# Kernel tuning notes

Hardware: AMD Instinct MI355X
Metric: run time of the kernel (lower is better)

## Reference

```python
import jax, jax.numpy as jnp
import numpy as np

N_PFAS, N_GW, N_SW = 20000, 100000, 20000
D_IN, D_OUT = 64, 128
E_PG, E_GP, E_SP, E_PS = 1600000, 1600000, 400000, 400000


def setup_inputs() -> dict:
    key = jax.random.key(0)
    ks = jax.random.split(key, 32)
    nrm = lambda k, shp, s=1.0: jax.random.normal(k, shp, jnp.float32) * s
    W = 0.05  # weight init scale
    inp = {
        # node features
        "x_pfas": nrm(ks[0], (N_PFAS, D_IN)),
        "x_gw": nrm(ks[1], (N_GW, D_IN)),
        "x_sw": nrm(ks[2], (N_SW, D_IN)),
        # edge indices per relation (src, dst)
        "ei_pg_src": jax.random.randint(ks[3], (E_PG,), 0, N_PFAS),
        "ei_pg_dst": jax.random.randint(ks[4], (E_PG,), 0, N_GW),
        "ei_gp_src": jax.random.randint(ks[5], (E_GP,), 0, N_GW),
        "ei_gp_dst": jax.random.randint(ks[6], (E_GP,), 0, N_PFAS),
        "ei_sp_src": jax.random.randint(ks[7], (E_SP,), 0, N_SW),
        "ei_sp_dst": jax.random.randint(ks[8], (E_SP,), 0, N_PFAS),
        "ei_ps_src": jax.random.randint(ks[9], (E_PS,), 0, N_PFAS),
        "ei_ps_dst": jax.random.randint(ks[10], (E_PS,), 0, N_SW),
        # SAGEConv params per relation: lin_l (neighbors, with bias), lin_r (root, no bias)
        "Wl_pg": nrm(ks[11], (D_IN, D_OUT), W), "Wr_pg": nrm(ks[12], (D_IN, D_OUT), W), "b_pg": jnp.zeros((D_OUT,), jnp.float32),
        "Wl_gp": nrm(ks[13], (D_IN, D_OUT), W), "Wr_gp": nrm(ks[14], (D_IN, D_OUT), W), "b_gp": jnp.zeros((D_OUT,), jnp.float32),
        "Wl_sp": nrm(ks[15], (D_IN, D_OUT), W), "Wr_sp": nrm(ks[16], (D_IN, D_OUT), W), "b_sp": jnp.zeros((D_OUT,), jnp.float32),
        "Wl_ps": nrm(ks[17], (D_IN, D_OUT), W), "Wr_ps": nrm(ks[18], (D_IN, D_OUT), W), "b_ps": jnp.zeros((D_OUT,), jnp.float32),
        # final linear head + PReLU
        "W_lin": nrm(ks[19], (D_OUT, 1), W), "b_lin": jnp.zeros((1,), jnp.float32),
        "alpha": jnp.full((1,), 0.25, jnp.float32),
    }
    return inp


def _sage(x_src, x_dst, src, dst, Wl, Wr, b, n_dst):
    # PyG SAGEConv: out = lin_l(mean_{j in N(i)} x_j) + lin_r(x_i)
    msg = x_src[src]                                   # [E, D_in] gather
    agg = jax.ops.segment_sum(msg, dst, num_segments=n_dst)        # [n_dst, D_in]
    cnt = jax.ops.segment_sum(jnp.ones(src.shape, x_src.dtype), dst, num_segments=n_dst)
    mean = agg / jnp.maximum(cnt, 1.0)[:, None]
    return mean @ Wl + x_dst @ Wr + b


def _prelu(y, a):
    return jnp.where(y > 0, y, a * y)


def reference(x_pfas, x_gw, x_sw, ei_pg_src, ei_pg_dst, ei_gp_src, ei_gp_dst,
              ei_sp_src, ei_sp_dst, ei_ps_src, ei_ps_dst,
              Wl_pg, Wr_pg, b_pg, Wl_gp, Wr_gp, b_gp, Wl_sp, Wr_sp, b_sp,
              Wl_ps, Wr_ps, b_ps, W_lin, b_lin, alpha):
    # HeteroConv with aggr='sum': pfas_sites receives from two relations (summed)
    h_gw = jax.nn.relu(_sage(x_pfas, x_gw, ei_pg_src, ei_pg_dst, Wl_pg, Wr_pg, b_pg, N_GW))
    h_pfas = jax.nn.relu(
        _sage(x_gw, x_pfas, ei_gp_src, ei_gp_dst, Wl_gp, Wr_gp, b_gp, N_PFAS)
        + _sage(x_sw, x_pfas, ei_sp_src, ei_sp_dst, Wl_sp, Wr_sp, b_sp, N_PFAS))
    h_sw = jax.nn.relu(_sage(x_pfas, x_sw, ei_ps_src, ei_ps_dst, Wl_ps, Wr_ps, b_ps, N_SW))
    out_gw = _prelu(h_gw @ W_lin + b_lin, alpha)   # [N_GW, 1]
    out_sw = _prelu(h_sw @ W_lin + b_lin, alpha)   # [N_SW, 1]
    return (h_pfas, out_gw, out_sw)
```

## Files before the change

### kernel.cpp

```cpp
#include <hip/hip_runtime.h>
#include <hip/hip_bf16.h>

#define N_PFAS 20000
#define N_GW   100000
#define N_SW   20000
#define N_SEG  160000
#define BASE_GW 0
#define BASE_GP 100000
#define BASE_SP 120000
#define BASE_PS 140000
#define NBIN 1250
#define NB_FILL 512
#define SORT_CAP 12288
#define N_XROW 140000

typedef __attribute__((ext_vector_type(8))) short short8;
typedef __attribute__((ext_vector_type(4))) float f32x4;
typedef __attribute__((ext_vector_type(2))) float f32x2;

__device__ __forceinline__ unsigned short f2bf(float f) {
    union { float f; unsigned int u; } v;
    v.f = f;
    unsigned int u = v.u;
    unsigned int r = (u + 0x7fffu + ((u >> 16) & 1u)) >> 16;
    return (unsigned short)r;
}
__device__ __forceinline__ float lo_bf(unsigned int v) {
    union { unsigned int u; float f; } w; w.u = v << 16; return w.f;
}
__device__ __forceinline__ float hi_bf(unsigned int v) {
    union { unsigned int u; float f; } w; w.u = v & 0xffff0000u; return w.f;
}

#if __has_builtin(__builtin_amdgcn_cvt_pk_f32_fp8) && __has_builtin(__builtin_amdgcn_cvt_pk_fp8_f32)
#define FP8_HW 1
__device__ __forceinline__ unsigned int enc_fp8x4(float4 v) {
    int r = __builtin_amdgcn_cvt_pk_fp8_f32(v.x, v.y, 0, false);
    r = __builtin_amdgcn_cvt_pk_fp8_f32(v.z, v.w, r, true);
    return (unsigned int)r;
}
__device__ __forceinline__ void dec_fp8x4v(unsigned int u, f32x2& lo, f32x2& hi) {
    lo = __builtin_amdgcn_cvt_pk_f32_fp8(u, false);
    hi = __builtin_amdgcn_cvt_pk_f32_fp8(u, true);
}
#else
__device__ __forceinline__ unsigned char enc1_e5m2(float f) {
    union { unsigned short u; _Float16 h; } cv;
    cv.h = (_Float16)f;
    unsigned int u = cv.u;
    unsigned int r = (u + 0x7Fu + ((u >> 8) & 1u)) >> 8;
    return (unsigned char)(r > 255u ? 255u : r);
}
__device__ __forceinline__ unsigned int enc_fp8x4(float4 v) {
    return (unsigned int)enc1_e5m2(v.x) | ((unsigned int)enc1_e5m2(v.y) << 8)
         | ((unsigned int)enc1_e5m2(v.z) << 16) | ((unsigned int)enc1_e5m2(v.w) << 24);
}
__device__ __forceinline__ float dec1_e5m2(unsigned int b) {
    union { unsigned short u; _Float16 h; } cv;
    cv.u = (unsigned short)(b << 8);
    return (float)cv.h;
}
__device__ __forceinline__ void dec_fp8x4v(unsigned int u, f32x2& lo, f32x2& hi) {
    lo.x = dec1_e5m2(u & 0xFF); lo.y = dec1_e5m2((u >> 8) & 0xFF);
    hi.x = dec1_e5m2((u >> 16) & 0xFF); hi.y = dec1_e5m2(u >> 24);
}
#endif

__device__ __forceinline__ void edge_lookup(int i,
    const int* __restrict__ s0, const int* __restrict__ d0, int E0,
    const int* __restrict__ s1, const int* __restrict__ d1, int E1,
    const int* __restrict__ s2, const int* __restrict__ d2, int E2,
    const int* __restrict__ s3, const int* __restrict__ d3,
    int& g, int& sv)
{
    if (i < E0)                { g = BASE_GW + d0[i];                 sv = s0 ? s0[i] : 0; }
    else if (i < E0 + E1)      { int j = i - E0;           g = BASE_GP + d1[j]; sv = s1 ? s1[j] : 0; }
    else if (i < E0 + E1 + E2) { int j = i - E0 - E1;      g = BASE_SP + d2[j]; sv = s2 ? s2[j] : 0; }
    else                       { int j = i - E0 - E1 - E2; g = BASE_PS + d3[j]; sv = s3 ? s3[j] : 0; }
}

__global__ void __launch_bounds__(1024)
count_cast(const int* __restrict__ d0, int E0, const int* __restrict__ d1, int E1,
           const int* __restrict__ d2, int E2, const int* __restrict__ d3, int E3,
           const float* __restrict__ xp, const float* __restrict__ xg,
           const float* __restrict__ xs, unsigned short* __restrict__ x16,
           unsigned int* __restrict__ x8, int* __restrict__ countMat)
{
    const int T0 = 20000 * 16, T1 = 120000 * 16, TT = N_XROW * 16;
    for (int i = blockIdx.x * 1024 + threadIdx.x; i < TT; i += NB_FILL * 1024) {
        float4 v;
        if (i < T0)      v = ((const float4*)xp)[i];
        else if (i < T1) v = ((const float4*)xg)[i - T0];
        else             v = ((const float4*)xs)[i - T1];
        ushort4 o;
        o.x = f2bf(v.x); o.y = f2bf(v.y); o.z = f2bf(v.z); o.w = f2bf(v.w);
        ((ushort4*)x16)[i] = o;
        if (x8) x8[i] = enc_fp8x4(v);
    }

    __shared__ int h[NBIN];
    for (int i = threadIdx.x; i < NBIN; i += 1024) h[i] = 0;
    __syncthreads();
    int total = E0 + E1 + E2 + E3;
    int CH = (total + NB_FILL - 1) / NB_FILL;
    int s = blockIdx.x * CH;
    int e = s + CH; if (e > total) e = total;
    for (int i0 = s + threadIdx.x * 4; i0 < e; i0 += 1024 * 4) {
        int gs[4];
        int m = e - i0; if (m > 4) m = 4;
        #pragma unroll
        for (int u = 0; u < 4; u++) {
            if (u < m) {
                int g, sv;
                edge_lookup(i0 + u, nullptr, d0, E0, nullptr, d1, E1,
                            nullptr, d2, E2, nullptr, d3, g, sv);
                gs[u] = g;
            }
        }
        #pragma unroll
        for (int u = 0; u < 4; u++)
            if (u < m) atomicAdd(&h[gs[u] >> 7], 1);
    }
    __syncthreads();
    for (int i = threadIdx.x; i < NBIN; i += 1024)
        countMat[blockIdx.x * NBIN + i] = h[i];
}

__global__ void __launch_bounds__(1024)
scan_part(const int* __restrict__ countMat, int* __restrict__ next,
          int* __restrict__ partials, int n)
{
    __shared__ int lds[1024];
    int i = blockIdx.x * 1024 + threadIdx.x;
    int v = 0;
    if (i < n) {
        int b = i >> 9, k = i & 511;
        v = countMat[k * NBIN + b];
    }
    lds[threadIdx.x] = v;
    __syncthreads();
    #pragma unroll
    for (int off = 1; off < 1024; off <<= 1) {
        int t = (threadIdx.x >= off) ? lds[threadIdx.x - off] : 0;
        __syncthreads();
        lds[threadIdx.x] += t;
        __syncthreads();
    }
    if (i < n) next[i] = lds[threadIdx.x] - v;
    if (threadIdx.x == 1023) partials[blockIdx.x] = lds[1023];
}

__device__ __forceinline__ int partials_prefix(const int* __restrict__ partials,
                                               int idx, int lane)
{
    int s = 0;
    for (int j = lane; j < idx; j += 64) s += partials[j];
    #pragma unroll
    for (int m = 32; m; m >>= 1) s += __shfl_xor(s, m);
    return s;
}

__global__ void __launch_bounds__(1024)
fill_bin(const int* __restrict__ s0, const int* __restrict__ d0, int E0,
         const int* __restrict__ s1, const int* __restrict__ d1, int E1,
         const int* __restrict__ s2, const int* __restrict__ d2, int E2,
         const int* __restrict__ s3, const int* __restrict__ d3, int E3,
         const int* __restrict__ next, const int* __restrict__ partials,
         int* __restrict__ edge_binned)
{
    __shared__ int cur[NBIN];
    __shared__ int sp[1024];
    {
        int t = threadIdx.x;
        int v = (t < 625) ? partials[t] : 0;
        sp[t] = v;
        __syncthreads();
        #pragma unroll
        for (int off = 1; off < 1024; off <<= 1) {
            int x = (t >= off) ? sp[t - off] : 0;
            __syncthreads();
            sp[t] += x;
            __syncthreads();
        }
        sp[t] -= v;
    }
    __syncthreads();
    for (int i = threadIdx.x; i < NBIN; i += 1024)
        cur[i] = next[i * NB_FILL + blockIdx.x] + sp[i >> 1];
    __syncthreads();
    int total = E0 + E1 + E2 + E3;
    int CH = (total + NB_FILL - 1) / NB_FILL;
    int s = blockIdx.x * CH;
    int e = s + CH; if (e > total) e = total;
    for (int i0 = s + threadIdx.x * 4; i0 < e; i0 += 1024 * 4) {
        int g[4], sv[4];
        int m = e - i0; if (m > 4) m = 4;
        #pragma unroll
        for (int u = 0; u < 4; u++)
            if (u < m) edge_lookup(i0 + u, s0, d0, E0, s1, d1, E1,
                                   s2, d2, E2, s3, d3, g[u], sv[u]);
        #pragma unroll
        for (int u = 0; u < 4; u++) {
            if (u < m) {
                int slot = atomicAdd(&cur[g[u] >> 7], 1);
                edge_binned[slot] = sv[u] | ((g[u] & 127) << 20);
            }
        }
    }
}

__global__ void __launch_bounds__(1024)
sort_agg(const int* __restrict__ next, const int* __restrict__ partials,
         const int* __restrict__ edge_binned,
         const unsigned int* __restrict__ x8,
         unsigned short* __restrict__ meanAll, int E_total)
{
    __shared__ int stage[SORT_CAP];
    __shared__ int cnt[128], basep[128], cur[128], lstart[128];
    int lane = threadIdx.x & 63;
    int b = (int)((blockIdx.x + 781u) % NBIN);
    int pA = partials_prefix(partials, b >> 1, lane);
    int start = next[b * NB_FILL] + pA;
    int end;
    if (b == NBIN - 1) end = E_total;
    else {
        int pB = pA + ((b & 1) ? partials[b >> 1] : 0);
        end = next[(b + 1) * NB_FILL] + pB;
    }
    int n = end - start;
    if (n > SORT_CAP) n = SORT_CAP;

    int vals[12];
    int nv = 0;
    if (threadIdx.x < 128) cnt[threadIdx.x] = 0;
    __syncthreads();
    for (int i = threadIdx.x; i < n; i += 1024) {
        int w = edge_binned[start + i];
        vals[nv++] = w;
        atomicAdd(&cnt[w >> 20], 1);
    }
    __syncthreads();
    if (threadIdx.x < 128) basep[threadIdx.x] = cnt[threadIdx.x];
    __syncthreads();
    #pragma unroll
    for (int off = 1; off < 128; off <<= 1) {
        int v = 0;
        if (threadIdx.x < 128 && threadIdx.x >= off) v = basep[threadIdx.x - off];
        __syncthreads();
        if (threadIdx.x < 128) basep[threadIdx.x] += v;
        __syncthreads();
    }
    if (threadIdx.x < 128) {
        int ex = basep[threadIdx.x] - cnt[threadIdx.x];
        cur[threadIdx.x] = ex;
        lstart[threadIdx.x] = ex;
    }
    __syncthreads();
    for (int u = 0; u < nv; u++) {
        int w = vals[u];
        int dl = w >> 20;
        int g = (b << 7) + dl;
        int rb = (g < BASE_GP) ? 0 : (g < BASE_SP) ? 20000
               : (g < BASE_PS) ? 120000 : 0;
        int slot = atomicAdd(&cur[dl], 1);
        stage[slot] = (w & 0xFFFFF) + rb;
    }
    __syncthreads();

    int wv = threadIdx.x >> 6;
    int h  = lane >> 5;
    int eq = (lane >> 3) & 3;
    int fc = lane & 7;
    int l32 = lane & 31;
    for (int it = 0; it < 4; it++) {
        int nl = 2 * (it * 16 + wv) + h;
        int s0 = lstart[nl];
        int c0 = cnt[nl];
        f32x2 a01 = {0.f,0.f}, a23 = {0.f,0.f}, a45 = {0.f,0.f}, a67 = {0.f,0.f};
        int j = 0;
        for (; j + 32 <= c0; j += 32) {
            int ev = stage[s0 + j + l32];
            #pragma unroll
            for (int t = 0; t < 8; t++) {
                int id = __shfl(ev, h * 32 + 4 * t + eq);
                uint2 v = *(const uint2*)(x8 + (((size_t)id) << 4) + fc * 2);
                f32x2 lo0, hi0, lo1, hi1;
                dec_fp8x4v(v.x, lo0, hi0);
                dec_fp8x4v(v.y, lo1, hi1);
                a01 += lo0; a23 += hi0; a45 += lo1; a67 += hi1;
            }
        }
        if (j < c0) {
            int blk = c0 - j;
            int ev = (l32 < blk) ? stage[s0 + j + l32] : 0;
            int ng = (blk + 3) >> 2;
            for (int t = 0; t < ng; t++) {
                int idx = 4 * t + eq;
                int id = __shfl(ev, h * 32 + idx);
                if (idx < blk) {
                    uint2 v = *(const uint2*)(x8 + (((size_t)id) << 4) + fc * 2);
                    f32x2 lo0, hi0, lo1, hi1;
                    dec_fp8x4v(v.x, lo0, hi0);
                    dec_fp8x4v(v.y, lo1, hi1);
                    a01 += lo0; a23 += hi0; a45 += lo1; a67 += hi1;
                }
            }
        }
        float f[8] = {a01.x, a01.y, a23.x, a23.y, a45.x, a45.y, a67.x, a67.y};
        #pragma unroll
        for (int r = 0; r < 8; r++) {
            f[r] += __shfl_xor(f[r], 8);
            f[r] += __shfl_xor(f[r], 16);
        }
        if (eq == 0) {
            float inv = 1.0f / (float)(c0 > 1 ? c0 : 1);
            ushort4 o0, o1;
            o0.x = f2bf(f[0] * inv); o0.y = f2bf(f[1] * inv);
            o0.z = f2bf(f[2] * inv); o0.w = f2bf(f[3] * inv);
            o1.x = f2bf(f[4] * inv); o1.y = f2bf(f[5] * inv);
            o1.z = f2bf(f[6] * inv); o1.w = f2bf(f[7] * inv);
            int gnode = (b << 7) + nl;
            ushort4* dst = (ushort4*)(meanAll + (size_t)gnode * 64 + fc * 8);
            dst[0] = o0;
            dst[1] = o1;
        }
    }
}

__global__ void __launch_bounds__(1024)
sort_bin(const int* __restrict__ next, const int* __restrict__ partials,
         int* __restrict__ edge_binned,
         int2* __restrict__ nodeMeta, int E_total)
{
    __shared__ int stage[SORT_CAP];
    __shared__ int cnt[128], basep[128], cur[128];
    int lane = threadIdx.x & 63;
    int b = (int)((blockIdx.x + 781u) % NBIN);
    int pA = partials_prefix(partials, b >> 1, lane);
    int start = next[b * NB_FILL] + pA;
    int end;
    if (b == NBIN - 1) end = E_total;
    else {
        int pB = pA + ((b & 1) ? partials[b >> 1] : 0);
        end = next[(b + 1) * NB_FILL] + pB;
    }
    int n = end - start;
    if (n > SORT_CAP) n = SORT_CAP;

    for (int i = threadIdx.x; i < n; i += 1024) stage[i] = edge_binned[start + i];
    if (threadIdx.x < 128) cnt[threadIdx.x] = 0;
    __syncthreads();
    for (int i = threadIdx.x; i < n; i += 1024) atomicAdd(&cnt[stage[i] >> 20], 1);
    __syncthreads();
    if (threadIdx.x < 128) basep[threadIdx.x] = cnt[threadIdx.x];
    __syncthreads();
    #pragma unroll
    for (int off = 1; off < 128; off <<= 1) {
        int v = 0;
        if (threadIdx.x < 128 && threadIdx.x >= off) v = basep[threadIdx.x - off];
        __syncthreads();
        if (threadIdx.x < 128) basep[threadIdx.x] += v;
        __syncthreads();
    }
    if (threadIdx.x < 128) {
        int ex = basep[threadIdx.x] - cnt[threadIdx.x];
        cur[threadIdx.x] = ex;
        int g = (b << 7) + threadIdx.x;
        nodeMeta[g] = make_int2(start + ex, cnt[threadIdx.x]);
    }
    __syncthreads();
    for (int i = threadIdx.x; i < n; i += 1024) {
        int w = stage[i];
        int dl = w >> 20;
        int g = (b << 7) + dl;
        int rb = (g < BASE_GP) ? 0 : (g < BASE_SP) ? 20000
               : (g < BASE_PS) ? 120000 : 0;
        int slot = atomicAdd(&cur[dl], 1);
        edge_binned[start + slot] = (w & 0xFFFFF) + rb;
    }
}

__global__ void __launch_bounds__(256)
agg_node16(const unsigned short* __restrict__ x16,
           const int2* __restrict__ nodeMeta,
           const int* __restrict__ edge_src, unsigned short* __restrict__ meanAll)
{
    int wlin = (blockIdx.x * blockDim.x + threadIdx.x) >> 6;
    int lane = threadIdx.x & 63;
    if (wlin >= N_SEG) return;
    int wid = (wlin < 60000) ? (BASE_GP + wlin) : (wlin - 60000);
    int quarter = lane >> 4;
    int fcol = lane & 15;
    int2 meta = nodeMeta[wid];
    int start = meta.x, cnt = meta.y;
    float a0 = 0.f, a1 = 0.f, a2 = 0.f, a3 = 0.f;
    int j = 0;
    while (j + 64 <= cnt) {
        int ev = edge_src[start + j + lane];
        #pragma unroll
        for (int t = 0; t < 16; t++) {
            int id = __shfl(ev, 4 * t + quarter);
            uint2 v = ((const uint2*)(x16 + (((size_t)id) << 6)))[fcol];
            a0 += lo_bf(v.x); a1 += hi_bf(v.x);
            a2 += lo_bf(v.y); a3 += hi_bf(v.y);
        }
        j += 64;
    }
    if (j < cnt) {
        int blk = cnt - j;
        int ev = (lane < blk) ? edge_src[start + j + lane] : 0;
        int ng = (blk + 3) >> 2;
        #pragma unroll 4
        for (int t = 0; t < ng; t++) {
            int idx = 4 * t + quarter;
            int id = __shfl(ev, idx);
            if (idx < blk) {
                uint2 v = ((const uint2*)(x16 + (((size_t)id) << 6)))[fcol];
                a0 += lo_bf(v.x); a1 += hi_bf(v.x);
                a2 += lo_bf(v.y); a3 += hi_bf(v.y);
            }
        }
    }
    a0 += __shfl_xor(a0, 16); a1 += __shfl_xor(a1, 16);
    a2 += __shfl_xor(a2, 16); a3 += __shfl_xor(a3, 16);
    a0 += __shfl_xor(a0, 32); a1 += __shfl_xor(a1, 32);
    a2 += __shfl_xor(a2, 32); a3 += __shfl_xor(a3, 32);
    if (quarter == 0) {
        float inv = 1.0f / (float)(cnt > 1 ? cnt : 1);
        ushort4 o;
        o.x = f2bf(a0 * inv); o.y = f2bf(a1 * inv);
        o.z = f2bf(a2 * inv); o.w = f2bf(a3 * inv);
        ((ushort4*)meanAll)[(size_t)wid * 16 + fcol] = o;
    }
}

__device__ __forceinline__ void
head_body(const unsigned short* __restrict__ x16r,
          const unsigned short* __restrict__ mean,
          const float* __restrict__ Wl, const float* __restrict__ Wr,
          const float* __restrict__ b, const float* __restrict__ Wlin,
          const float* __restrict__ b_lin, const float* __restrict__ alpha,
          float* __restrict__ out, int N, int bid, int nblocks,
          unsigned short* __restrict__ smem)
{
    unsigned short* sW = smem;

    for (int i = threadIdx.x; i < 64 * 128; i += 256) {
        int k = i >> 7, col = i & 127;
        sW[col * 136 + k]      = f2bf(Wl[k * 128 + col]);
        sW[col * 136 + 64 + k] = f2bf(Wr[k * 128 + col]);
    }

    int lane = threadIdx.x & 63;
    int wid  = threadIdx.x >> 6;
    int c    = lane & 15;
    int quad = lane >> 4;
    float wl_c[8], b_c[8];
    #pragma unroll
    for (int t = 0; t < 8; t++) {
        wl_c[t] = Wlin[t * 16 + c];
        b_c[t]  = b[t * 16 + c];
    }
    float blin = b_lin[0], al = alpha[0];
    __syncthreads();

    int ntiles = (N + 63) >> 6;
    for (int tile = bid; tile < ntiles; tile += nblocks) {
        int base = tile << 6;
        int node = base + wid * 16 + c;
        bool valid = node < N;
        const unsigned short* mrow = mean + (size_t)node * 64;
        const unsigned short* xrow = x16r + (size_t)node * 64;

        f32x4 acc[8] = {};
        #pragma unroll
        for (int step = 0; step < 4; step++) {
            short8 a = {};
            if (valid) {
                const unsigned short* src = (step < 2)
                    ? (mrow + step * 32 + quad * 8)
                    : (xrow + (step - 2) * 32 + quad * 8);
                a = *(const short8*)src;
            }
            #pragma unroll
            for (int t = 0; t < 8; t++) {
                short8 bb = *(const short8*)&sW[(t * 16 + c) * 136 + step * 32 + quad * 8];
                acc[t] = __builtin_amdgcn_mfma_f32_16x16x32_bf16(a, bb, acc[t], 0, 0, 0);
            }
        }

        float p[4] = {0.f, 0.f, 0.f, 0.f};
        #pragma unroll
        for (int t = 0; t < 8; t++) {
            #pragma unroll
            for (int r = 0; r < 4; r++) {
                float h = fmaxf(acc[t][r] + b_c[t], 0.0f);
                p[r] += h * wl_c[t];
            }
        }
        #pragma unroll
        for (int m = 1; m < 16; m <<= 1) {
            #pragma unroll
            for (int r = 0; r < 4; r++) p[r] += __shfl_xor(p[r], m);
        }
        if (c == 0) {
            #pragma unroll
            for (int r = 0; r < 4; r++) {
                int onode = base + wid * 16 + quad * 4 + r;
                if (onode < N) {
                    float y = p[r] + blin;
                    out[onode] = y > 0.0f ? y : al * y;
                }
            }
        }
    }
}

__device__ __forceinline__ void
pfas_body(const unsigned short* __restrict__ x16p,
          const unsigned short* __restrict__ meanGP,
          const unsigned short* __restrict__ meanSP,
          const float* __restrict__ WlGP, const float* __restrict__ WrGP,
          const float* __restrict__ bGP,
          const float* __restrict__ WlSP, const float* __restrict__ WrSP,
          const float* __restrict__ bSP,
          float* __restrict__ out, int N, int bid, int nblocks,
          unsigned short* __restrict__ smem)
{
    unsigned short* sW = smem;

    for (int i = threadIdx.x; i < 64 * 128; i += 256) {
        int k = i >> 7, col = i & 127;
        sW[col * 200 + k]       = f2bf(WlGP[k * 128 + col]);
        sW[col * 200 + 64 + k]  = f2bf(WlSP[k * 128 + col]);
        sW[col * 200 + 128 + k] = f2bf(WrGP[k * 128 + col] + WrSP[k * 128 + col]);
    }

    int lane = threadIdx.x & 63;
    int wid  = threadIdx.x >> 6;
    int c    = lane & 15;
    int quad = lane >> 4;
    int rg   = (wid & 1) * 16;
    int cg   = (wid >> 1) * 4;
    float b_c[4];
    #pragma unroll
    for (int t = 0; t < 4; t++)
        b_c[t] = bGP[(cg + t) * 16 + c] + bSP[(cg + t) * 16 + c];
    __syncthreads();

    int ntiles = (N + 31) >> 5;
    for (int tile = bid; tile < ntiles; tile += nblocks) {
        int base = tile << 5;
        int node = base + rg + c;
        bool valid = node < N;
        const unsigned short* grow = meanGP + (size_t)node * 64;
        const unsigned short* srow = meanSP + (size_t)node * 64;
        const unsigned short* xrow = x16p + (size_t)node * 64;

        f32x4 acc[4] = {};
        #pragma unroll
        for (int step = 0; step < 6; step++) {
            short8 a = {};
            if (valid) {
                const unsigned short* src = (step < 2)
                    ? (grow + step * 32 + quad * 8)
                    : (step < 4) ? (srow + (step - 2) * 32 + quad * 8)
                                 : (xrow + (step - 4) * 32 + quad * 8);
                a = *(const short8*)src;
            }
            #pragma unroll
            for (int t = 0; t < 4; t++) {
                short8 bb = *(const short8*)&sW[((cg + t) * 16 + c) * 200 + step * 32 + quad * 8];
                acc[t] = __builtin_amdgcn_mfma_f32_16x16x32_bf16(a, bb, acc[t], 0, 0, 0);
            }
        }

        #pragma unroll
        for (int t = 0; t < 4; t++) {
            int col = (cg + t) * 16 + c;
            #pragma unroll
            for (int r = 0; r < 4; r++) {
                int onode = base + rg + quad * 4 + r;
                if (onode < N) {
                    float h = fmaxf(acc[t][r] + b_c[t], 0.0f);
                    out[(size_t)onode * 128 + col] = h;
                }
            }
        }
    }
}

__global__ void __launch_bounds__(256)
node_mfma(const unsigned short* __restrict__ x16,
          const unsigned short* __restrict__ meanAll,
          const float* __restrict__ Wl_pg, const float* __restrict__ Wr_pg,
          const float* __restrict__ b_pg,
          const float* __restrict__ Wl_ps, const float* __restrict__ Wr_ps,
          const float* __restrict__ b_ps,
          const float* __restrict__ Wl_gp, const float* __restrict__ Wr_gp,
          const float* __restrict__ b_gp,
          const float* __restrict__ Wl_sp, const float* __restrict__ Wr_sp,
          const float* __restrict__ b_sp,
          const float* __restrict__ W_lin, const float* __restrict__ b_lin,
          const float* __restrict__ alpha,
          float* __restrict__ out_gw, float* __restrict__ out_sw,
          float* __restrict__ out_pfas)
{
    __shared__ __align__(16) unsigned short smem[25600];
    int bx = blockIdx.x;
    if (bx < 512) {
        head_body(x16 + (size_t)20000 * 64, meanAll + (size_t)BASE_GW * 64,
                  Wl_pg, Wr_pg, b_pg, W_lin, b_lin, alpha,
                  out_gw, N_GW, bx, 512, smem);
    } else if (bx < 672) {
        head_body(x16 + (size_t)120000 * 64, meanAll + (size_t)BASE_PS * 64,
                  Wl_ps, Wr_ps, b_ps, W_lin, b_lin, alpha,
                  out_sw, N_SW, bx - 512, 160, smem);
    } else {
        pfas_body(x16, meanAll + (size_t)BASE_GP * 64, meanAll + (size_t)BASE_SP * 64,
                  Wl_gp, Wr_gp, b_gp, Wl_sp, Wr_sp, b_sp,
                  out_pfas, N_PFAS, bx - 672, 224, smem);
    }
}

extern "C" void kernel_launch(void* const* d_in, const int* in_sizes, int n_in,
                              void* d_out, int out_size, void* d_ws, size_t ws_size,
                              hipStream_t stream)
{
    const float* x_pfas = (const float*)d_in[0];
    const float* x_gw   = (const float*)d_in[1];
    const float* x_sw   = (const float*)d_in[2];
    const int* pg_src = (const int*)d_in[3];
    const int* pg_dst = (const int*)d_in[4];
    const int* gp_src = (const int*)d_in[5];
    const int* gp_dst = (const int*)d_in[6];
    const int* sp_src = (const int*)d_in[7];
    const int* sp_dst = (const int*)d_in[8];
    const int* ps_src = (const int*)d_in[9];
    const int* ps_dst = (const int*)d_in[10];
    const float* Wl_pg = (const float*)d_in[11];
    const float* Wr_pg = (const float*)d_in[12];
    const float* b_pg  = (const float*)d_in[13];
    const float* Wl_gp = (const float*)d_in[14];
    const float* Wr_gp = (const float*)d_in[15];
    const float* b_gp  = (const float*)d_in[16];
    const float* Wl_sp = (const float*)d_in[17];
    const float* Wr_sp = (const float*)d_in[18];
    const float* b_sp  = (const float*)d_in[19];
    const float* Wl_ps = (const float*)d_in[20];
    const float* Wr_ps = (const float*)d_in[21];
    const float* b_ps  = (const float*)d_in[22];
    const float* W_lin = (const float*)d_in[23];
    const float* b_lin = (const float*)d_in[24];
    const float* alpha = (const float*)d_in[25];

    float* out = (float*)d_out;
    float* out_pfas = out;
    float* out_gw   = out + (size_t)N_PFAS * 128;
    float* out_sw   = out_gw + N_GW;

    int E_PG = in_sizes[3];
    int E_GP = in_sizes[5];
    int E_SP = in_sizes[7];
    int E_PS = in_sizes[9];
    int E_total = E_PG + E_GP + E_SP + E_PS;

    unsigned short* meanAll = (unsigned short*)d_ws;
    int* countMat  = (int*)(meanAll + (size_t)N_SEG * 64);
    int2* nodeMeta = (int2*)countMat;
    int* next      = countMat + NB_FILL * NBIN;
    int* partials  = next + NB_FILL * NBIN;
    int* edge_binned = partials + 1024;
    unsigned short* x16 = (unsigned short*)(edge_binned + E_total);
    unsigned int* x8 = (unsigned int*)(x16 + (size_t)N_XROW * 64);
    size_t needed8 = (size_t)((char*)(x8 + (size_t)N_XROW * 16) - (char*)d_ws);
    bool use8 = (ws_size >= needed8);

    const int SCAN_N  = NB_FILL * NBIN;
    const int SCAN_NB = SCAN_N / 1024;

    count_cast<<<NB_FILL, 1024, 0, stream>>>(pg_dst, E_PG, gp_dst, E_GP,
                                             sp_dst, E_SP, ps_dst, E_PS,
                                             x_pfas, x_gw, x_sw, x16,
                                             use8 ? x8 : (unsigned int*)nullptr,
                                             countMat);

    scan_part<<<SCAN_NB, 1024, 0, stream>>>(countMat, next, partials, SCAN_N);

    fill_bin<<<NB_FILL, 1024, 0, stream>>>(pg_src, pg_dst, E_PG,
                                           gp_src, gp_dst, E_GP,
                                           sp_src, sp_dst, E_SP,
                                           ps_src, ps_dst, E_PS,
                                           next, partials, edge_binned);

    if (use8) {
        sort_agg<<<NBIN, 1024, 0, stream>>>(next, partials, edge_binned,
                                            x8, meanAll, E_total);
    } else {
        sort_bin<<<NBIN, 1024, 0, stream>>>(next, partials, edge_binned,
                                            nodeMeta, E_total);
        agg_node16<<<(N_SEG * 64 + 255) / 256, 256, 0, stream>>>(x16, nodeMeta,
                                                                 edge_binned, meanAll);
    }

    node_mfma<<<896, 256, 0, stream>>>(x16, meanAll,
                                       Wl_pg, Wr_pg, b_pg,
                                       Wl_ps, Wr_ps, b_ps,
                                       Wl_gp, Wr_gp, b_gp,
                                       Wl_sp, Wr_sp, b_sp,
                                       W_lin, b_lin, alpha,
                                       out_gw, out_sw, out_pfas);
}
```

Measured before the change: 290.1 us.

## Replace two-level bin sort with per-node global-atomic counting sort

The bucketed CSR build is replaced. Before, a per-block LDS histogram over 1250 bins was followed by an in-LDS sort per bin. Now there is a direct per-destination-node histogram using global atomics, a flat scan plus fixup, and a scatter fill that atomically claims a slot per node. The separate sort_agg stage becomes a grid-stride agg8 kernel that reads neighbor ids straight from the CSR array. This removes the second sort pass and its LDS staging. In exchange it does 3.2M global atomics twice with random addresses, and the edge order within each node becomes nondeterministic.

```diff
diff --git a/kernel.cpp b/kernel.cpp
--- a/kernel.cpp
+++ b/kernel.cpp
@@ -9,10 +9,9 @@
 #define BASE_GP 100000
 #define BASE_SP 120000
 #define BASE_PS 140000
-#define NBIN 1250
 #define NB_FILL 512
-#define SORT_CAP 12288
 #define N_XROW 140000
+#define NBLK_SCAN 157
 
 typedef __attribute__((ext_vector_type(8))) short short8;
 typedef __attribute__((ext_vector_type(4))) float f32x4;
@@ -24,12 +23,6 @@
     unsigned int u = v.u;
     unsigned int r = (u + 0x7fffu + ((u >> 16) & 1u)) >> 16;
     return (unsigned short)r;
-}
-__device__ __forceinline__ float lo_bf(unsigned int v) {
-    union { unsigned int u; float f; } w; w.u = v << 16; return w.f;
-}
-__device__ __forceinline__ float hi_bf(unsigned int v) {
-    union { unsigned int u; float f; } w; w.u = v & 0xffff0000u; return w.f;
 }
 
 #if __has_builtin(__builtin_amdgcn_cvt_pk_f32_fp8) && __has_builtin(__builtin_amdgcn_cvt_pk_fp8_f32)
@@ -66,17 +59,11 @@
 }
 #endif
 
-__device__ __forceinline__ void edge_lookup(int i,
-    const int* __restrict__ s0, const int* __restrict__ d0, int E0,
-    const int* __restrict__ s1, const int* __restrict__ d1, int E1,
-    const int* __restrict__ s2, const int* __restrict__ d2, int E2,
-    const int* __restrict__ s3, const int* __restrict__ d3,
-    int& g, int& sv)
-{
-    if (i < E0)                { g = BASE_GW + d0[i];                 sv = s0 ? s0[i] : 0; }
-    else if (i < E0 + E1)      { int j = i - E0;           g = BASE_GP + d1[j]; sv = s1 ? s1[j] : 0; }
-    else if (i < E0 + E1 + E2) { int j = i - E0 - E1;      g = BASE_SP + d2[j]; sv = s2 ? s2[j] : 0; }
-    else                       { int j = i - E0 - E1 - E2; g = BASE_PS + d3[j]; sv = s3 ? s3[j] : 0; }
+__global__ void __launch_bounds__(1024)
+zero_hist(int* __restrict__ hist)
+{
+    int i = blockIdx.x * 1024 + threadIdx.x;
+    if (i < N_SEG) hist[i] = 0;
 }
 
 __global__ void __launch_bounds__(1024)
@@ -84,7 +71,7 @@
            const int* __restrict__ d2, int E2, const int* __restrict__ d3, int E3,
            const float* __restrict__ xp, const float* __restrict__ xg,
            const float* __restrict__ xs, unsigned short* __restrict__ x16,
-           unsigned int* __restrict__ x8, int* __restrict__ countMat)
+           unsigned int* __restrict__ x8, int* __restrict__ hist)
 {
     const int T0 = 20000 * 16, T1 = 120000 * 16, TT = N_XROW * 16;
     for (int i = blockIdx.x * 1024 + threadIdx.x; i < TT; i += NB_FILL * 1024) {
@@ -95,48 +82,37 @@
         ushort4 o;
         o.x = f2bf(v.x); o.y = f2bf(v.y); o.z = f2bf(v.z); o.w = f2bf(v.w);
         ((ushort4*)x16)[i] = o;
-        if (x8) x8[i] = enc_fp8x4(v);
-    }
-
-    __shared__ int h[NBIN];
-    for (int i = threadIdx.x; i < NBIN; i += 1024) h[i] = 0;
-    __syncthreads();
+        x8[i] = enc_fp8x4(v);
+    }
+
     int total = E0 + E1 + E2 + E3;
-    int CH = (total + NB_FILL - 1) / NB_FILL;
-    int s = blockIdx.x * CH;
-    int e = s + CH; if (e > total) e = total;
-    for (int i0 = s + threadIdx.x * 4; i0 < e; i0 += 1024 * 4) {
-        int gs[4];
-        int m = e - i0; if (m > 4) m = 4;
-        #pragma unroll
-        for (int u = 0; u < 4; u++) {
-            if (u < m) {
-                int g, sv;
-                edge_lookup(i0 + u, nullptr, d0, E0, nullptr, d1, E1,
-                            nullptr, d2, E2, nullptr, d3, g, sv);
-                gs[u] = g;
-            }
-        }
-        #pragma unroll
-        for (int u = 0; u < 4; u++)
-            if (u < m) atomicAdd(&h[gs[u] >> 7], 1);
-    }
-    __syncthreads();
-    for (int i = threadIdx.x; i < NBIN; i += 1024)
-        countMat[blockIdx.x * NBIN + i] = h[i];
+    for (int i0 = (blockIdx.x * 1024 + threadIdx.x) * 4; i0 < total;
+         i0 += NB_FILL * 1024 * 4) {
+        const int* dp; int base, j;
+        if (i0 < E0)                { dp = d0; base = BASE_GW; j = i0; }
+        else if (i0 < E0 + E1)      { dp = d1; base = BASE_GP; j = i0 - E0; }
+        else if (i0 < E0 + E1 + E2) { dp = d2; base = BASE_SP; j = i0 - E0 - E1; }
+        else                        { dp = d3; base = BASE_PS; j = i0 - E0 - E1 - E2; }
+        if (i0 + 4 <= total) {
+            int4 d = ((const int4*)dp)[j >> 2];
+            atomicAdd(&hist[base + d.x], 1);
+            atomicAdd(&hist[base + d.y], 1);
+            atomicAdd(&hist[base + d.z], 1);
+            atomicAdd(&hist[base + d.w], 1);
+        } else {
+            for (int u = 0; i0 + u < total; u++)
+                atomicAdd(&hist[base + dp[j + u]], 1);
+        }
+    }
 }
 
 __global__ void __launch_bounds__(1024)
-scan_part(const int* __restrict__ countMat, int* __restrict__ next,
+scan_part(const int* __restrict__ hist, int* __restrict__ next,
           int* __restrict__ partials, int n)
 {
     __shared__ int lds[1024];
     int i = blockIdx.x * 1024 + threadIdx.x;
-    int v = 0;
-    if (i < n) {
-        int b = i >> 9, k = i & 511;
-        v = countMat[k * NBIN + b];
-    }
+    int v = (i < n) ? hist[i] : 0;
     lds[threadIdx.x] = v;
     __syncthreads();
     #pragma unroll
@@ -161,125 +137,73 @@
 }
 
 __global__ void __launch_bounds__(1024)
-fill_bin(const int* __restrict__ s0, const int* __restrict__ d0, int E0,
-         const int* __restrict__ s1, const int* __restrict__ d1, int E1,
-         const int* __restrict__ s2, const int* __restrict__ d2, int E2,
-         const int* __restrict__ s3, const int* __restrict__ d3, int E3,
-         const int* __restrict__ next, const int* __restrict__ partials,
-         int* __restrict__ edge_binned)
-{
-    __shared__ int cur[NBIN];
-    __shared__ int sp[1024];
-    {
-        int t = threadIdx.x;
-        int v = (t < 625) ? partials[t] : 0;
-        sp[t] = v;
-        __syncthreads();
-        #pragma unroll
-        for (int off = 1; off < 1024; off <<= 1) {
-            int x = (t >= off) ? sp[t - off] : 0;
-            __syncthreads();
-            sp[t] += x;
-            __syncthreads();
-        }
-        sp[t] -= v;
-    }
-    __syncthreads();
-    for (int i = threadIdx.x; i < NBIN; i += 1024)
-        cur[i] = next[i * NB_FILL + blockIdx.x] + sp[i >> 1];
-    __syncthreads();
+fixup(const int* __restrict__ next, const int* __restrict__ partials,
+      int* __restrict__ off, int* __restrict__ cur, int n)
+{
+    int lane = threadIdx.x & 63;
+    int s = partials_prefix(partials, blockIdx.x, lane);
+    int i = blockIdx.x * 1024 + threadIdx.x;
+    if (i < n) {
+        int o = next[i] + s;
+        off[i] = o;
+        cur[i] = o;
+    }
+}
+
+__global__ void __launch_bounds__(1024)
+fill_bin(const int* __restrict__ s0_, const int* __restrict__ d0, int E0,
+         const int* __restrict__ s1_, const int* __restrict__ d1, int E1,
+         const int* __restrict__ s2_, const int* __restrict__ d2, int E2,
+         const int* __restrict__ s3_, const int* __restrict__ d3, int E3,
+         int* __restrict__ cur, int* __restrict__ eb)
+{
     int total = E0 + E1 + E2 + E3;
-    int CH = (total + NB_FILL - 1) / NB_FILL;
-    int s = blockIdx.x * CH;
-    int e = s + CH; if (e > total) e = total;
-    for (int i0 = s + threadIdx.x * 4; i0 < e; i0 += 1024 * 4) {
-        int g[4], sv[4];
-        int m = e - i0; if (m > 4) m = 4;
-        #pragma unroll
-        for (int u = 0; u < 4; u++)
-            if (u < m) edge_lookup(i0 + u, s0, d0, E0, s1, d1, E1,
-                                   s2, d2, E2, s3, d3, g[u], sv[u]);
-        #pragma unroll
-        for (int u = 0; u < 4; u++) {
-            if (u < m) {
-                int slot = atomicAdd(&cur[g[u] >> 7], 1);
-                edge_binned[slot] = sv[u] | ((g[u] & 127) << 20);
-            }
-        }
-    }
-}
-
-__global__ void __launch_bounds__(1024)
-sort_agg(const int* __restrict__ next, const int* __restrict__ partials,
-         const int* __restrict__ edge_binned,
-         const unsigned int* __restrict__ x8,
-         unsigned short* __restrict__ meanAll, int E_total)
-{
-    __shared__ int stage[SORT_CAP];
-    __shared__ int cnt[128], basep[128], cur[128], lstart[128];
+    for (int i0 = (blockIdx.x * 1024 + threadIdx.x) * 4; i0 < total;
+         i0 += NB_FILL * 1024 * 4) {
+        const int *sp, *dp; int base, rb, j;
+        if (i0 < E0)                { sp = s0_; dp = d0; base = BASE_GW; rb = 0;      j = i0; }
+        else if (i0 < E0 + E1)      { sp = s1_; dp = d1; base = BASE_GP; rb = 20000;  j = i0 - E0; }
+        else if (i0 < E0 + E1 + E2) { sp = s2_; dp = d2; base = BASE_SP; rb = 120000; j = i0 - E0 - E1; }
+        else                        { sp = s3_; dp = d3; base = BASE_PS; rb = 0;      j = i0 - E0 - E1 - E2; }
+        if (i0 + 4 <= total) {
+            int4 s = ((const int4*)sp)[j >> 2];
+            int4 d = ((const int4*)dp)[j >> 2];
+            int sl;
+            sl = atomicAdd(&cur[base + d.x], 1); eb[sl] = rb + s.x;
+            sl = atomicAdd(&cur[base + d.y], 1); eb[sl] = rb + s.y;
+            sl = atomicAdd(&cur[base + d.z], 1); eb[sl] = rb + s.z;
+            sl = atomicAdd(&cur[base + d.w], 1); eb[sl] = rb + s.w;
+        } else {
+            for (int u = 0; i0 + u < total; u++) {
+                int sl = atomicAdd(&cur[base + dp[j + u]], 1);
+                eb[sl] = rb + sp[j + u];
+            }
+        }
+    }
+}
+
+__global__ void __launch_bounds__(256)
+agg8(const int* __restrict__ off, const int* __restrict__ hist,
+     const int* __restrict__ eb, const unsigned int* __restrict__ x8,
+     unsigned short* __restrict__ meanAll)
+{
     int lane = threadIdx.x & 63;
-    int b = (int)((blockIdx.x + 781u) % NBIN);
-    int pA = partials_prefix(partials, b >> 1, lane);
-    int start = next[b * NB_FILL] + pA;
-    int end;
-    if (b == NBIN - 1) end = E_total;
-    else {
-        int pB = pA + ((b & 1) ? partials[b >> 1] : 0);
-        end = next[(b + 1) * NB_FILL] + pB;
-    }
-    int n = end - start;
-    if (n > SORT_CAP) n = SORT_CAP;
-
-    int vals[12];
-    int nv = 0;
-    if (threadIdx.x < 128) cnt[threadIdx.x] = 0;
-    __syncthreads();
-    for (int i = threadIdx.x; i < n; i += 1024) {
-        int w = edge_binned[start + i];
-        vals[nv++] = w;
-        atomicAdd(&cnt[w >> 20], 1);
-    }
-    __syncthreads();
-    if (threadIdx.x < 128) basep[threadIdx.x] = cnt[threadIdx.x];
-    __syncthreads();
-    #pragma unroll
-    for (int off = 1; off < 128; off <<= 1) {
-        int v = 0;
-        if (threadIdx.x < 128 && threadIdx.x >= off) v = basep[threadIdx.x - off];
-        __syncthreads();
-        if (threadIdx.x < 128) basep[threadIdx.x] += v;
-        __syncthreads();
-    }
-    if (threadIdx.x < 128) {
-        int ex = basep[threadIdx.x] - cnt[threadIdx.x];
-        cur[threadIdx.x] = ex;
-        lstart[threadIdx.x] = ex;
-    }
-    __syncthreads();
-    for (int u = 0; u < nv; u++) {
-        int w = vals[u];
-        int dl = w >> 20;
-        int g = (b << 7) + dl;
-        int rb = (g < BASE_GP) ? 0 : (g < BASE_SP) ? 20000
-               : (g < BASE_PS) ? 120000 : 0;
-        int slot = atomicAdd(&cur[dl], 1);
-        stage[slot] = (w & 0xFFFFF) + rb;
-    }
-    __syncthreads();
-
-    int wv = threadIdx.x >> 6;
-    int h  = lane >> 5;
-    int eq = (lane >> 3) & 3;
-    int fc = lane & 7;
+    int wv = (blockIdx.x * 256 + threadIdx.x) >> 6;
+    int nw = (gridDim.x * 256) >> 6;
+    int h   = lane >> 5;
+    int eq  = (lane >> 3) & 3;
+    int fc  = lane & 7;
     int l32 = lane & 31;
-    for (int it = 0; it < 4; it++) {
-        int nl = 2 * (it * 16 + wv) + h;
-        int s0 = lstart[nl];
-        int c0 = cnt[nl];
+    for (int pr = wv; pr < N_SEG / 2; pr += nw) {
+        int p = pr * 2;
+        int g = (p < 60000) ? p + 100000 : p - 60000;
+        int n0 = g + h;
+        int s0 = off[n0];
+        int c0 = hist[n0];
         f32x2 a01 = {0.f,0.f}, a23 = {0.f,0.f}, a45 = {0.f,0.f}, a67 = {0.f,0.f};
         int j = 0;
         for (; j + 32 <= c0; j += 32) {
-            int ev = stage[s0 + j + l32];
+            int ev = eb[s0 + j + l32];
             #pragma unroll
             for (int t = 0; t < 8; t++) {
                 int id = __shfl(ev, h * 32 + 4 * t + eq);
@@ -292,7 +216,7 @@
         }
         if (j < c0) {
             int blk = c0 - j;
-            int ev = (l32 < blk) ? stage[s0 + j + l32] : 0;
+            int ev = (l32 < blk) ? eb[s0 + j + l32] : 0;
             int ng = (blk + 3) >> 2;
             for (int t = 0; t < ng; t++) {
                 int idx = 4 * t + eq;
@@ -319,118 +243,10 @@
             o0.z = f2bf(f[2] * inv); o0.w = f2bf(f[3] * inv);
             o1.x = f2bf(f[4] * inv); o1.y = f2bf(f[5] * inv);
             o1.z = f2bf(f[6] * inv); o1.w = f2bf(f[7] * inv);
-            int gnode = (b << 7) + nl;
-            ushort4* dst = (ushort4*)(meanAll + (size_t)gnode * 64 + fc * 8);
+            ushort4* dst = (ushort4*)(meanAll + (size_t)n0 * 64 + fc * 8);
             dst[0] = o0;
             dst[1] = o1;
         }
-    }
-}
-
-__global__ void __launch_bounds__(1024)
-sort_bin(const int* __restrict__ next, const int* __restrict__ partials,
-         int* __restrict__ edge_binned,
-         int2* __restrict__ nodeMeta, int E_total)
-{
-    __shared__ int stage[SORT_CAP];
-    __shared__ int cnt[128], basep[128], cur[128];
-    int lane = threadIdx.x & 63;
-    int b = (int)((blockIdx.x + 781u) % NBIN);
-    int pA = partials_prefix(partials, b >> 1, lane);
-    int start = next[b * NB_FILL] + pA;
-    int end;
-    if (b == NBIN - 1) end = E_total;
-    else {
-        int pB = pA + ((b & 1) ? partials[b >> 1] : 0);
-        end = next[(b + 1) * NB_FILL] + pB;
-    }
-    int n = end - start;
-    if (n > SORT_CAP) n = SORT_CAP;
-
-    for (int i = threadIdx.x; i < n; i += 1024) stage[i] = edge_binned[start + i];
-    if (threadIdx.x < 128) cnt[threadIdx.x] = 0;
-    __syncthreads();
-    for (int i = threadIdx.x; i < n; i += 1024) atomicAdd(&cnt[stage[i] >> 20], 1);
-    __syncthreads();
-    if (threadIdx.x < 128) basep[threadIdx.x] = cnt[threadIdx.x];
-    __syncthreads();
-    #pragma unroll
-    for (int off = 1; off < 128; off <<= 1) {
-        int v = 0;
-        if (threadIdx.x < 128 && threadIdx.x >= off) v = basep[threadIdx.x - off];
-        __syncthreads();
-        if (threadIdx.x < 128) basep[threadIdx.x] += v;
-        __syncthreads();
-    }
-    if (threadIdx.x < 128) {
-        int ex = basep[threadIdx.x] - cnt[threadIdx.x];
-        cur[threadIdx.x] = ex;
-        int g = (b << 7) + threadIdx.x;
-        nodeMeta[g] = make_int2(start + ex, cnt[threadIdx.x]);
-    }
-    __syncthreads();
-    for (int i = threadIdx.x; i < n; i += 1024) {
-        int w = stage[i];
-        int dl = w >> 20;
-        int g = (b << 7) + dl;
-        int rb = (g < BASE_GP) ? 0 : (g < BASE_SP) ? 20000
-               : (g < BASE_PS) ? 120000 : 0;
-        int slot = atomicAdd(&cur[dl], 1);
-        edge_binned[start + slot] = (w & 0xFFFFF) + rb;
-    }
-}
-
-__global__ void __launch_bounds__(256)
-agg_node16(const unsigned short* __restrict__ x16,
-           const int2* __restrict__ nodeMeta,
-           const int* __restrict__ edge_src, unsigned short* __restrict__ meanAll)
-{
-    int wlin = (blockIdx.x * blockDim.x + threadIdx.x) >> 6;
-    int lane = threadIdx.x & 63;
-    if (wlin >= N_SEG) return;
-    int wid = (wlin < 60000) ? (BASE_GP + wlin) : (wlin - 60000);
-    int quarter = lane >> 4;
-    int fcol = lane & 15;
-    int2 meta = nodeMeta[wid];
-    int start = meta.x, cnt = meta.y;
-    float a0 = 0.f, a1 = 0.f, a2 = 0.f, a3 = 0.f;
-    int j = 0;
-    while (j + 64 <= cnt) {
-        int ev = edge_src[start + j + lane];
-        #pragma unroll
-        for (int t = 0; t < 16; t++) {
-            int id = __shfl(ev, 4 * t + quarter);
-            uint2 v = ((const uint2*)(x16 + (((size_t)id) << 6)))[fcol];
-            a0 += lo_bf(v.x); a1 += hi_bf(v.x);
-            a2 += lo_bf(v.y); a3 += hi_bf(v.y);
-        }
-        j += 64;
-    }
-    if (j < cnt) {
-        int blk = cnt - j;
-        int ev = (lane < blk) ? edge_src[start + j + lane] : 0;
-        int ng = (blk + 3) >> 2;
-        #pragma unroll 4
-        for (int t = 0; t < ng; t++) {
-            int idx = 4 * t + quarter;
-            int id = __shfl(ev, idx);
-            if (idx < blk) {
-                uint2 v = ((const uint2*)(x16 + (((size_t)id) << 6)))[fcol];
-                a0 += lo_bf(v.x); a1 += hi_bf(v.x);
-                a2 += lo_bf(v.y); a3 += hi_bf(v.y);
-            }
-        }
-    }
-    a0 += __shfl_xor(a0, 16); a1 += __shfl_xor(a1, 16);
-    a2 += __shfl_xor(a2, 16); a3 += __shfl_xor(a3, 16);
-    a0 += __shfl_xor(a0, 32); a1 += __shfl_xor(a1, 32);
-    a2 += __shfl_xor(a2, 32); a3 += __shfl_xor(a3, 32);
-    if (quarter == 0) {
-        float inv = 1.0f / (float)(cnt > 1 ? cnt : 1);
-        ushort4 o;
-        o.x = f2bf(a0 * inv); o.y = f2bf(a1 * inv);
-        o.z = f2bf(a2 * inv); o.w = f2bf(a3 * inv);
-        ((ushort4*)meanAll)[(size_t)wid * 16 + fcol] = o;
     }
 }
 
@@ -666,42 +482,32 @@
     int E_total = E_PG + E_GP + E_SP + E_PS;
 
     unsigned short* meanAll = (unsigned short*)d_ws;
-    int* countMat  = (int*)(meanAll + (size_t)N_SEG * 64);
-    int2* nodeMeta = (int2*)countMat;
-    int* next      = countMat + NB_FILL * NBIN;
-    int* partials  = next + NB_FILL * NBIN;
-    int* edge_binned = partials + 1024;
+    int* hist     = (int*)(meanAll + (size_t)N_SEG * 64);
+    int* next     = hist + N_SEG;
+    int* off      = next + N_SEG;
+    int* cur      = off + N_SEG;
+    int* partials = cur + N_SEG;
+    int* edge_binned = partials + 256;
     unsigned short* x16 = (unsigned short*)(edge_binned + E_total);
     unsigned int* x8 = (unsigned int*)(x16 + (size_t)N_XROW * 64);
-    size_t needed8 = (size_t)((char*)(x8 + (size_t)N_XROW * 16) - (char*)d_ws);
-    bool use8 = (ws_size >= needed8);
-
-    const int SCAN_N  = NB_FILL * NBIN;
-    const int SCAN_NB = SCAN_N / 1024;
+
+    zero_hist<<<NBLK_SCAN, 1024, 0, stream>>>(hist);
 
     count_cast<<<NB_FILL, 1024, 0, stream>>>(pg_dst, E_PG, gp_dst, E_GP,
                                              sp_dst, E_SP, ps_dst, E_PS,
-                                             x_pfas, x_gw, x_sw, x16,
-                                             use8 ? x8 : (unsigned int*)nullptr,
-                                             countMat);
-
-    scan_part<<<SCAN_NB, 1024, 0, stream>>>(countMat, next, partials, SCAN_N);
+                                             x_pfas, x_gw, x_sw, x16, x8, hist);
+
+    scan_part<<<NBLK_SCAN, 1024, 0, stream>>>(hist, next, partials, N_SEG);
+
+    fixup<<<NBLK_SCAN, 1024, 0, stream>>>(next, partials, off, cur, N_SEG);
 
     fill_bin<<<NB_FILL, 1024, 0, stream>>>(pg_src, pg_dst, E_PG,
                                            gp_src, gp_dst, E_GP,
                                            sp_src, sp_dst, E_SP,
                                            ps_src, ps_dst, E_PS,
-                                           next, partials, edge_binned);
-
-    if (use8) {
-        sort_agg<<<NBIN, 1024, 0, stream>>>(next, partials, edge_binned,
-                                            x8, meanAll, E_total);
-    } else {
-        sort_bin<<<NBIN, 1024, 0, stream>>>(next, partials, edge_binned,
-                                            nodeMeta, E_total);
-        agg_node16<<<(N_SEG * 64 + 255) / 256, 256, 0, stream>>>(x16, nodeMeta,
-                                                                 edge_binned, meanAll);
-    }
+                                           cur, edge_binned);
+
+    agg8<<<2048, 256, 0, stream>>>(off, hist, edge_binned, x8, meanAll);
 
     node_mfma<<<896, 256, 0, stream>>>(x16, meanAll,
                                        Wl_pg, Wr_pg, b_pg,
```

After: 707.4 us. +143.8%, slower.
